# Performance work log

Measured on AMD Instinct MI355X. Metric: run time of the kernel, lower is better.

## Reference

```python
import jax, jax.numpy as jnp
import numpy as np

S, B, C, H, E, V, T = 196, 64, 1024, 1024, 512, 32000, 20


def setup_inputs() -> dict:
    key = jax.random.key(0)
    ks = jax.random.split(key, 16)

    def w(k, shape, fan_in):
        return (jax.random.normal(k, shape, jnp.float32) / np.sqrt(fan_in)).astype(jnp.float32)

    emb_W = w(ks[2], (V, E), E).at[0].set(0.0)  # padding_idx=0
    return {
        'ctx': jax.random.normal(ks[0], (S, B, C), jnp.float32),
        'y': jax.random.randint(ks[1], (T, B), 0, V, jnp.int32),
        'emb_W': emb_W,
        'att_ctx2ctx': w(ks[3], (C, C), C),
        'att_hid2ctx': w(ks[4], (H, C), H),
        'att_mlp': w(ks[5], (C,), C),
        'gru_W_ih': w(ks[6], (3 * H, E + C), E + C),
        'gru_b_ih': jnp.zeros((3 * H,), jnp.float32),
        'gru_W_hh': w(ks[7], (3 * H, H), H),
        'gru_b_hh': jnp.zeros((3 * H,), jnp.float32),
        'hid2out_W': w(ks[8], (E, H), H),
        'hid2out_b': jnp.zeros((E,), jnp.float32),
        'out_ctx_W': w(ks[9], (E, C), C),
        'out_ctx_b': jnp.zeros((E,), jnp.float32),
        'out2prob_W': w(ks[10], (V, E), E),
        'out2prob_b': jnp.zeros((V,), jnp.float32),
    }


def reference(ctx, y, emb_W, att_ctx2ctx, att_hid2ctx, att_mlp,
              gru_W_ih, gru_b_ih, gru_W_hh, gru_b_hh,
              hid2out_W, hid2out_b, out_ctx_W, out_ctx_b,
              out2prob_W, out2prob_b):
    hidden = gru_W_hh.shape[1]
    y_emb = emb_W[y]                                        # [T, B, E]
    ctx_proj = jnp.einsum('sbc,cm->sbm', ctx, att_ctx2ctx)  # precompute ctx2ctx(ctx)

    def gru_cell(x, h):
        gi = x @ gru_W_ih.T + gru_b_ih
        gh = h @ gru_W_hh.T + gru_b_hh
        i_r, i_z, i_n = jnp.split(gi, 3, axis=-1)
        h_r, h_z, h_n = jnp.split(gh, 3, axis=-1)
        r = jax.nn.sigmoid(i_r + h_r)
        z = jax.nn.sigmoid(i_z + h_z)
        n = jnp.tanh(i_n + r * h_n)
        return (1.0 - z) * n + z * h

    def step(h, inp):
        y_t, tgt = inp                                      # [B,E], [B]
        # MLP attention over source positions S
        scores = jnp.einsum('sbm,m->sb', jnp.tanh(ctx_proj + (h @ att_hid2ctx)[None]), att_mlp)
        alpha = jax.nn.softmax(scores, axis=0)              # [S, B]
        z_t = jnp.einsum('sb,sbc->bc', alpha, ctx)          # [B, C]
        ht = gru_cell(jnp.concatenate([y_t, z_t], axis=-1), h)
        logit = jnp.tanh(ht @ hid2out_W.T + hid2out_b)      # hid2out (tanh FF)
        logit = logit + y_t                                 # prev2out
        logit = logit + z_t @ out_ctx_W.T + out_ctx_b       # ctx2out
        log_p = jax.nn.log_softmax(jnp.tanh(logit) @ out2prob_W.T + out2prob_b, axis=-1)
        mask = (tgt != 0).astype(log_p.dtype)               # NLLLoss ignore_index=0, sum
        nll = -jnp.sum(jnp.take_along_axis(log_p, tgt[:, None], axis=1)[:, 0] * mask)
        return ht, nll

    h0 = jnp.zeros((y.shape[1], hidden), ctx.dtype)         # dec_init='zero'
    _, nlls = jax.lax.scan(step, h0, (y_emb[:-1], y[1:]))
    return jnp.sum(nlls)
```

## Files before the change

kernel.cpp:

```cpp
#include <hip/hip_runtime.h>
#include <math.h>

#define TS_ 19

typedef float f32x4 __attribute__((ext_vector_type(4)));
typedef short s16x8 __attribute__((ext_vector_type(8)));
typedef unsigned short us;
typedef unsigned char uc;

__device__ __forceinline__ float sigmoidf_(float x) { return 1.f / (1.f + __expf(-x)); }

__device__ __forceinline__ float fast_tanh(float x) {
    float ax = fabsf(x);
    float e = __expf(-2.f * ax);
    float r = (1.f - e) * __builtin_amdgcn_rcpf(1.f + e);
    return copysignf(r, x);
}

__device__ __forceinline__ us f2b(float x) {
    union { float f; unsigned u; } v; v.f = x;
    unsigned r = v.u + 0x7fffu + ((v.u >> 16) & 1u);
    return (us)(r >> 16);
}
__device__ __forceinline__ float b2f(us u) {
    union { unsigned u; float f; } v; v.u = ((unsigned)u) << 16; return v.f;
}
__device__ __forceinline__ uc f2e4m3(float x) {
    return (uc)(__builtin_amdgcn_cvt_pk_fp8_f32(x, 0.f, 0, false) & 0xff);
}

#define MFMA(a, b, c) __builtin_amdgcn_mfma_f32_16x16x32_bf16((a), (b), (c), 0, 0, 0)
#define MFMA8(a, b, c) __builtin_amdgcn_mfma_f32_16x16x32_fp8_fp8((a), (b), (c), 0, 0, 0)

__device__ __forceinline__ f32x4 zero4() { return (f32x4){0.f, 0.f, 0.f, 0.f}; }

__device__ __forceinline__ f32x4 wg16(const us* ap, const us* bp, int nk, f32x4 acc) {
#pragma unroll 4
    for (int k = 0; k < nk; k += 32)
        acc = MFMA(*(const s16x8*)(ap + k), *(const s16x8*)(bp + k), acc);
    return acc;
}

__device__ __forceinline__ void gload_lds16(const void* g, void* l) {
    __builtin_amdgcn_global_load_lds(
        (const __attribute__((address_space(1))) unsigned int*)g,
        (__attribute__((address_space(3))) unsigned int*)l, 16, 0, 0);
}

__global__ __launch_bounds__(256) void k_cvt(const float* __restrict__ in,
                                             us* __restrict__ out, long n) {
    long i = ((long)blockIdx.x * 256 + threadIdx.x) * 4;
    long stride = (long)gridDim.x * 1024;
    for (; i < n; i += stride) {
        float4 v = *(const float4*)(in + i);
        ushort4 o = { f2b(v.x), f2b(v.y), f2b(v.z), f2b(v.w) };
        *(ushort4*)(out + i) = o;
    }
}

__global__ __launch_bounds__(256) void k_cvt8(const float* __restrict__ in,
                                              uc* __restrict__ out, long n) {
    long i = ((long)blockIdx.x * 256 + threadIdx.x) * 8;
    long stride = (long)gridDim.x * 2048;
    for (; i < n; i += stride) {
        float4 v0 = *(const float4*)(in + i);
        float4 v1 = *(const float4*)(in + i + 4);
        int lo = __builtin_amdgcn_cvt_pk_fp8_f32(v0.x, v0.y, 0, false);
        lo = __builtin_amdgcn_cvt_pk_fp8_f32(v0.z, v0.w, lo, true);
        int hi = __builtin_amdgcn_cvt_pk_fp8_f32(v1.x, v1.y, 0, false);
        hi = __builtin_amdgcn_cvt_pk_fp8_f32(v1.z, v1.w, hi, true);
        int2 o = { lo, hi };
        *(int2*)(out + i) = o;
    }
}

__global__ void k_tcvt(const float* __restrict__ in, us* __restrict__ out) {
    __shared__ float tile[32][33];
    int bx = blockIdx.x * 32, by = blockIdx.y * 32;
    int x = threadIdx.x, y0 = threadIdx.y;
    for (int yy = y0; yy < 32; yy += 8) tile[yy][x] = in[(by + yy) * 1024 + bx + x];
    __syncthreads();
    for (int yy = y0; yy < 32; yy += 8) out[(bx + yy) * 1024 + by + x] = f2b(tile[x][yy]);
}

__global__ __launch_bounds__(256) void k_yemb(const int* __restrict__ y,
                                              const float* __restrict__ embW,
                                              us* __restrict__ xc) {
    int t = blockIdx.x >> 6, b = blockIdx.x & 63;
    int row = y[t * 64 + b];
    const float* src = embW + (long)row * 512;
    us* dst = xc + (long)(t * 64 + b) * 2560;
    for (int e = threadIdx.x; e < 512; e += 256) dst[e] = f2b(src[e]);
}

__global__ __launch_bounds__(256) void k_prepw(const float* __restrict__ Wih,
                                               const float* __restrict__ Whh,
                                               us* __restrict__ Wg) {
    int n = blockIdx.x, tid = threadIdx.x;
    int cl = n >> 10;
    if (cl < 2) {
        long base = (long)n * 2560;
        const float* wi = Wih + (long)n * 1536;
        const float* wh = Whh + (long)n * 1024;
        for (int k = tid; k < 1536; k += 256) Wg[base + k] = f2b(wi[k]);
        for (int k = tid; k < 1024; k += 256) Wg[base + 1536 + k] = f2b(wh[k]);
    } else if (cl == 2) {
        long base = 5242880L + (long)(n - 2048) * 1536;
        const float* wi = Wih + (long)n * 1536;
        for (int k = tid; k < 1536; k += 256) Wg[base + k] = f2b(wi[k]);
    } else {
        long base = 6815744L + (long)(n - 3072) * 1024;
        const float* wh = Whh + (long)(n - 1024) * 1024;
        for (int k = tid; k < 1024; k += 256) Wg[base + k] = f2b(wh[k]);
    }
}

__global__ __launch_bounds__(256) void k_gemm(const us* __restrict__ A,
                                              const us* __restrict__ Bt,
                                              us* __restrict__ Cb) {
    __shared__ us As[8192], Bs[8192];
    int tid = threadIdx.x, lane = tid & 63, w = tid >> 6;
    int mr = lane & 15, kb = lane >> 4;
    int bm = blockIdx.x % 98, bn = blockIdx.x / 98;
    long m0 = (long)bm * 128;
    int n0 = bn * 128;
    int wr = w >> 1, wc = w & 1;
    int srow = w * 32 + (lane >> 3);
    int ib = (lane & 7) * 16;

    f32x4 acc[4][4];
#pragma unroll
    for (int i = 0; i < 4; i++)
#pragma unroll
        for (int j = 0; j < 4; j++) acc[i][j] = zero4();

    for (int kt = 0; kt < 16; ++kt) {
        int k0 = kt * 64;
        __syncthreads();
#pragma unroll
        for (int c = 0; c < 4; ++c) {
            int r = srow + c * 8;
            int sw = (ib ^ ((r & 7) << 4)) >> 1;
            gload_lds16(A + (m0 + r) * 1024 + k0 + sw, &As[w * 2048 + c * 512]);
            gload_lds16(Bt + (long)(n0 + r) * 1024 + k0 + sw, &Bs[w * 2048 + c * 512]);
        }
        __syncthreads();
#pragma unroll
        for (int ks = 0; ks < 2; ++ks) {
            s16x8 af[4], bf[4];
#pragma unroll
            for (int mt = 0; mt < 4; ++mt) {
                int r = wr * 64 + mt * 16 + mr;
                af[mt] = *(const s16x8*)&As[(r * 128 + ((ks * 64 + kb * 16) ^ ((r & 7) << 4))) >> 1];
            }
#pragma unroll
            for (int nt = 0; nt < 4; ++nt) {
                int r = wc * 64 + nt * 16 + mr;
                bf[nt] = *(const s16x8*)&Bs[(r * 128 + ((ks * 64 + kb * 16) ^ ((r & 7) << 4))) >> 1];
            }
#pragma unroll
            for (int mt = 0; mt < 4; ++mt)
#pragma unroll
                for (int nt = 0; nt < 4; ++nt)
                    acc[mt][nt] = MFMA(af[mt], bf[nt], acc[mt][nt]);
        }
    }
#pragma unroll
    for (int mt = 0; mt < 4; ++mt)
#pragma unroll
        for (int nt = 0; nt < 4; ++nt)
#pragma unroll
            for (int j = 0; j < 4; ++j)
                Cb[(m0 + wr * 64 + mt * 16 + kb * 4 + j) * 1024 +
                   n0 + wc * 64 + nt * 16 + mr] = f2b(acc[mt][nt][j]);
}

__global__ __launch_bounds__(256) void k_hproj(const us* __restrict__ hcur,
                                               const us* __restrict__ attbf,
                                               float* __restrict__ hpp) {
    int tid = threadIdx.x, lane = tid & 63, w = tid >> 6;
    int vn0 = (blockIdx.x >> 1) * 16, kc = blockIdx.x & 1;
    int m0 = w * 16, mr = lane & 15, kb = lane >> 4;
    const us* ap = hcur + (long)(m0 + mr) * 1024 + kc * 512 + kb * 8;
    const us* bp = attbf + (long)(vn0 + mr) * 1024 + kc * 512 + kb * 8;
    f32x4 acc = wg16(ap, bp, 512, zero4());
#pragma unroll
    for (int j = 0; j < 4; ++j)
        hpp[(long)kc * 65536 + (long)(m0 + kb * 4 + j) * 1024 + vn0 + mr] = acc[j];
}

__global__ __launch_bounds__(1024) void k_scores(const us* __restrict__ cpb,
                                                 const float* __restrict__ hpp,
                                                 const float* __restrict__ mlp,
                                                 float* __restrict__ scores) {
    __shared__ float hp[1024];
    __shared__ float ml[1024];
    int tid = threadIdx.x;
    int b = blockIdx.x >> 2, sq = blockIdx.x & 3;
    hp[tid] = hpp[(long)b * 1024 + tid] + hpp[65536 + (long)b * 1024 + tid];
    ml[tid] = mlp[tid];
    __syncthreads();
    int wv = tid >> 6, lane = tid & 63;
    int s0 = sq * 49;
    for (int s = s0 + wv; s < s0 + 49; s += 16) {
        const us* cp = cpb + (long)(s * 64 + b) * 1024 + lane * 16;
        s16x8 c0 = *(const s16x8*)cp;
        s16x8 c1 = *(const s16x8*)(cp + 8);
        int e0 = lane * 16;
        float acc = 0.f;
#pragma unroll
        for (int j = 0; j < 8; ++j)
            acc += fast_tanh(b2f((us)c0[j]) + hp[e0 + j]) * ml[e0 + j];
#pragma unroll
        for (int j = 0; j < 8; ++j)
            acc += fast_tanh(b2f((us)c1[j]) + hp[e0 + 8 + j]) * ml[e0 + 8 + j];
#pragma unroll
        for (int off = 32; off; off >>= 1) acc += __shfl_xor(acc, off, 64);
        if (lane == 0) scores[b * 196 + s] = acc;
    }
}

__global__ __launch_bounds__(512) void k_z(const float* __restrict__ scores,
                                           const us* __restrict__ ctxbf,
                                           us* __restrict__ xc, int t) {
    __shared__ float red[512];
    __shared__ float als[196];
    __shared__ float zp[256];
    int tid = threadIdx.x, b = blockIdx.x >> 2, ch = blockIdx.x & 3;
    const float* sc = scores + b * 196;
    float lm = (tid < 196) ? sc[tid] : -1e30f;
    red[tid] = lm; __syncthreads();
    for (int st = 256; st; st >>= 1) { if (tid < st) red[tid] = fmaxf(red[tid], red[tid + st]); __syncthreads(); }
    float m = red[0]; __syncthreads();
    float ls = (tid < 196) ? __expf(sc[tid] - m) : 0.f;
    red[tid] = ls; __syncthreads();
    for (int st = 256; st; st >>= 1) { if (tid < st) red[tid] += red[tid + st]; __syncthreads(); }
    float inv = 1.f / red[0];
    if (tid < 196) als[tid] = ls * inv;
    __syncthreads();
    int c = ch * 256 + (tid & 255);
    int sh = tid >> 8;
    const us* cp = ctxbf + (long)b * 1024 + c;
    float a0 = 0.f;
    int sb = sh * 98;
#pragma unroll 4
    for (int s = sb; s < sb + 98; s += 2) {
        a0 += als[s] * b2f(cp[(long)s * 65536]) +
              als[s + 1] * b2f(cp[(long)(s + 1) * 65536]);
    }
    if (sh) zp[tid & 255] = a0;
    __syncthreads();
    if (!sh) {
        a0 += zp[tid & 255];
        xc[(long)(t * 64 + b) * 2560 + 512 + c] = f2b(a0);
    }
}

__global__ __launch_bounds__(512) void k_gruh2(us* __restrict__ xc,
                                               const us* __restrict__ Wg,
                                               const float* __restrict__ bih,
                                               const float* __restrict__ bhh,
                                               float* __restrict__ hf32,
                                               us* __restrict__ ht_all, int t) {
    __shared__ float lg[2048];
    int tid = threadIdx.x, lane = tid & 63, w = tid >> 6;
    int mr = lane & 15, kb = lane >> 4;
    int g = w >> 1, kh = w & 1;
    int mq = blockIdx.x & 3, jt = blockIdx.x >> 2;
    int m0 = mq * 16, j0 = jt * 16;
    const us* xr = xc + (long)t * 163840 + (long)(m0 + mr) * 2560;

    f32x4 acc = zero4();
    if (g == 0) {
        acc = wg16(xr + kh * 1280 + kb * 8,
                   Wg + (long)(j0 + mr) * 2560 + kh * 1280 + kb * 8, 1280, acc);
    } else if (g == 1) {
        acc = wg16(xr + kh * 1280 + kb * 8,
                   Wg + (long)(1024 + j0 + mr) * 2560 + kh * 1280 + kb * 8, 1280, acc);
    } else if (g == 2) {
        acc = wg16(xr + kh * 768 + kb * 8,
                   Wg + 5242880L + (long)(j0 + mr) * 1536 + kh * 768 + kb * 8, 768, acc);
    } else {
        acc = wg16(xr + 1536 + kh * 512 + kb * 8,
                   Wg + 6815744L + (long)(j0 + mr) * 1024 + kh * 512 + kb * 8, 512, acc);
    }
#pragma unroll
    for (int j = 0; j < 4; ++j)
        lg[(g * 2 + kh) * 256 + (kb * 4 + j) * 16 + mr] = acc[j];
    __syncthreads();

    if (tid < 256) {
        int ml = tid >> 4, jj = tid & 15;
        int b = m0 + ml, j = j0 + jj;
        float gr = lg[0 * 256 + ml * 16 + jj] + lg[1 * 256 + ml * 16 + jj];
        float gz = lg[2 * 256 + ml * 16 + jj] + lg[3 * 256 + ml * 16 + jj];
        float gi = lg[4 * 256 + ml * 16 + jj] + lg[5 * 256 + ml * 16 + jj];
        float gh = lg[6 * 256 + ml * 16 + jj] + lg[7 * 256 + ml * 16 + jj];
        float r  = sigmoidf_(gr + bih[j] + bhh[j]);
        float zz = sigmoidf_(gz + bih[1024 + j] + bhh[1024 + j]);
        float n  = fast_tanh(gi + bih[2048 + j] + r * (gh + bhh[2048 + j]));
        float h = (1.f - zz) * n + zz * hf32[b * 1024 + j];
        hf32[b * 1024 + j] = h;
        us hb = f2b(h);
        ht_all[(long)((t + 1) * 64 + b) * 1024 + j] = hb;
        if (t < TS_ - 1) xc[(long)((t + 1) * 64 + b) * 2560 + 1536 + j] = hb;
    }
}

__global__ __launch_bounds__(256) void k_outb(const us* __restrict__ ht_all,
                                              const us* __restrict__ xc,
                                              const us* __restrict__ h2obf,
                                              const float* __restrict__ h2ob,
                                              const us* __restrict__ octxbf,
                                              const float* __restrict__ octxb,
                                              us* __restrict__ obf_all,
                                              uc* __restrict__ obf8) {
    int tid = threadIdx.x, lane = tid & 63, w = tid >> 6;
    int mr = lane & 15, kb = lane >> 4;
    int m0 = blockIdx.x * 64;
    int n0 = blockIdx.y * 64;
    int e = n0 + w * 16 + mr;
    const us* bb1 = h2obf + (long)e * 1024 + kb * 8;
    const us* bb2 = octxbf + (long)e * 1024 + kb * 8;
    const us* ab1 = ht_all + (long)(64 + m0 + mr) * 1024 + kb * 8;
    const us* ab2 = xc + (long)(m0 + mr) * 2560 + 512 + kb * 8;

    f32x4 a1[4], a2[4];
#pragma unroll
    for (int i = 0; i < 4; i++) { a1[i] = zero4(); a2[i] = zero4(); }

#pragma unroll 2
    for (int k0 = 0; k0 < 1024; k0 += 32) {
        s16x8 b1 = *(const s16x8*)(bb1 + k0);
        s16x8 b2 = *(const s16x8*)(bb2 + k0);
#pragma unroll
        for (int mt = 0; mt < 4; ++mt) {
            a1[mt] = MFMA(*(const s16x8*)(ab1 + mt * 16384 + k0), b1, a1[mt]);
            a2[mt] = MFMA(*(const s16x8*)(ab2 + mt * 40960 + k0), b2, a2[mt]);
        }
    }
    float b1v = h2ob[e], b2v = octxb[e];
#pragma unroll
    for (int mt = 0; mt < 4; ++mt)
#pragma unroll
        for (int j = 0; j < 4; ++j) {
            long row = m0 + mt * 16 + kb * 4 + j;
            float ye = b2f(xc[row * 2560 + e]);
            float val = fast_tanh(fast_tanh(a1[mt][j] + b1v) + ye + a2[mt][j] + b2v);
            obf_all[(row << 9) + e] = f2b(val);
            obf8[(row << 9) + e] = f2e4m3(val);
        }
}

__global__ __launch_bounds__(256) void k_vocab8(const uc* __restrict__ obf8,
                                                const uc* __restrict__ o2p8,
                                                const float* __restrict__ o2pb,
                                                float* __restrict__ pm,
                                                float* __restrict__ ps) {
    __shared__ uc As[8192], Bs[8192];
    int tid = threadIdx.x, lane = tid & 63, w = tid >> 6;
    int mr = lane & 15, kb = lane >> 4;
    int xq = blockIdx.x & 7, idx = blockIdx.x >> 3;
    int nb = xq * 32 + idx / 10, mb = idx % 10;
    int m0 = mb * 128, n0 = nb * 128;
    int wr = w >> 1, wc = w & 1;
    int srow = w * 32 + (lane >> 2);
    int ib = (lane & 3) * 16;

    f32x4 acc[4][4];
#pragma unroll
    for (int i = 0; i < 4; i++)
#pragma unroll
        for (int j = 0; j < 4; j++) acc[i][j] = zero4();

    for (int kt = 0; kt < 8; ++kt) {
        int k0 = kt * 64;
        __syncthreads();
#pragma unroll
        for (int c = 0; c < 2; ++c) {
            int r = srow + c * 16;
            int sw = ib ^ ((r & 6) << 3);
            gload_lds16(obf8 + (long)(m0 + r) * 512 + k0 + sw, &As[w * 2048 + c * 1024]);
            gload_lds16(o2p8 + (long)(n0 + r) * 512 + k0 + sw, &Bs[w * 2048 + c * 1024]);
        }
        __syncthreads();
#pragma unroll
        for (int ks = 0; ks < 2; ++ks) {
            long af[4], bf[4];
#pragma unroll
            for (int mt = 0; mt < 4; ++mt) {
                int r = wr * 64 + mt * 16 + mr;
                af[mt] = *(const long*)&As[r * 64 + ((ks * 32 + kb * 8) ^ ((r & 6) << 3))];
            }
#pragma unroll
            for (int nt = 0; nt < 4; ++nt) {
                int r = wc * 64 + nt * 16 + mr;
                bf[nt] = *(const long*)&Bs[r * 64 + ((ks * 32 + kb * 8) ^ ((r & 6) << 3))];
            }
#pragma unroll
            for (int mt = 0; mt < 4; ++mt)
#pragma unroll
                for (int nt = 0; nt < 4; ++nt)
                    acc[mt][nt] = MFMA8(af[mt], bf[nt], acc[mt][nt]);
        }
    }

    int n0w = n0 + wc * 64;
    float bv[4];
#pragma unroll
    for (int nt = 0; nt < 4; ++nt) {
        int vn = n0w + nt * 16 + mr;
        bv[nt] = (vn < 32000) ? o2pb[vn] : -1e30f;
    }
#pragma unroll
    for (int mt = 0; mt < 4; ++mt)
#pragma unroll
        for (int j = 0; j < 4; ++j) {
            float x0 = acc[mt][0][j] + bv[0];
            float x1 = acc[mt][1][j] + bv[1];
            float x2 = acc[mt][2][j] + bv[2];
            float x3 = acc[mt][3][j] + bv[3];
            float m = fmaxf(fmaxf(x0, x1), fmaxf(x2, x3));
            float s = __expf(x0 - m) + __expf(x1 - m) + __expf(x2 - m) + __expf(x3 - m);
#pragma unroll
            for (int off = 1; off <= 8; off <<= 1) {
                float mo = __shfl_xor(m, off, 64), so = __shfl_xor(s, off, 64);
                float nm = fmaxf(m, mo);
                s = s * __expf(m - nm) + so * __expf(mo - nm);
                m = nm;
            }
            if (mr == 0) {
                int row = m0 + wr * 64 + mt * 16 + kb * 4 + j;
                pm[(long)(nb * 2 + wc) * 1280 + row] = m;
                ps[(long)(nb * 2 + wc) * 1280 + row] = s;
            }
        }
}

__global__ __launch_bounds__(64) void k_lseb(const float* __restrict__ pm,
                                             const float* __restrict__ ps,
                                             const us* __restrict__ obf_all,
                                             const float* __restrict__ o2pW,
                                             const float* __restrict__ o2pb,
                                             const int* __restrict__ y,
                                             float* __restrict__ out) {
    int r = blockIdx.x, lane = threadIdx.x;
    int t = r >> 6, b = r & 63;
    int tgt = y[(t + 1) * 64 + b];
    float m = -1e30f, s = 0.f;
    for (int p = lane; p < 512; p += 64) {
        float mi = pm[(long)p * 1280 + r], si = ps[(long)p * 1280 + r];
        float nm = fmaxf(m, mi);
        s = s * __expf(m - nm) + si * __expf(mi - nm);
        m = nm;
    }
#pragma unroll
    for (int off = 32; off; off >>= 1) {
        float mo = __shfl_xor(m, off, 64), so = __shfl_xor(s, off, 64);
        float nm = fmaxf(m, mo);
        s = s * __expf(m - nm) + so * __expf(mo - nm);
        m = nm;
    }
    float d = 0.f;
    const float* wr = o2pW + (long)tgt * 512;
#pragma unroll
    for (int k = 0; k < 8; ++k)
        d += b2f(obf_all[(long)r * 512 + lane + k * 64]) * wr[lane + k * 64];
#pragma unroll
    for (int off = 32; off; off >>= 1) d += __shfl_xor(d, off, 64);
    if (lane == 0 && tgt != 0)
        atomicAdd(out, (m + __logf(s)) - (d + o2pb[tgt]));
}

extern "C" void kernel_launch(void* const* d_in, const int* in_sizes, int n_in,
                              void* d_out, int out_size, void* d_ws, size_t ws_size,
                              hipStream_t stream) {
    const float* ctx     = (const float*)d_in[0];
    const int*   y       = (const int*)d_in[1];
    const float* embW    = (const float*)d_in[2];
    const float* att_c2c = (const float*)d_in[3];
    const float* att_h2c = (const float*)d_in[4];
    const float* mlp     = (const float*)d_in[5];
    const float* Wih     = (const float*)d_in[6];
    const float* bih     = (const float*)d_in[7];
    const float* Whh     = (const float*)d_in[8];
    const float* bhh     = (const float*)d_in[9];
    const float* h2oW    = (const float*)d_in[10];
    const float* h2ob    = (const float*)d_in[11];
    const float* octxW   = (const float*)d_in[12];
    const float* octxb   = (const float*)d_in[13];
    const float* o2pW    = (const float*)d_in[14];
    const float* o2pb    = (const float*)d_in[15];
    float* out = (float*)d_out;

    char* base = (char*)d_ws;
    us* ctxbf   = (us*)base; base += 25690112L;
    us* cpbf    = (us*)base; base += 25690112L;
    us* c2cT    = (us*)base; base += 2097152L;
    us* attbf   = (us*)base; base += 2097152L;
    us* Wg      = (us*)base; base += 15728640L;
    us* h2obf   = (us*)base; base += 1048576L;
    us* octxbf  = (us*)base; base += 1048576L;
    uc* o2p8    = (uc*)base; base += 16777216L;
    us* xc      = (us*)base; base += 6225920L;
    us* ht_all  = (us*)base; base += 2621440L;
    us* obf_all = (us*)base; base += 1310720L;
    uc* obf8    = (uc*)base; base += 655360L;
    float* hf32   = (float*)base; base += 262144L;
    float* hpp    = (float*)base; base += 524288L;
    float* scb    = (float*)base; base += 50176L;
    float* pm   = (float*)cpbf;
    float* ps   = pm + 655360L;

    (void)hipMemsetAsync(d_out, 0, sizeof(float), stream);
    (void)hipMemsetAsync(hf32, 0, 262144, stream);
    (void)hipMemsetAsync(ht_all, 0, 131072, stream);
    (void)hipMemsetAsync(obf_all + 1216L * 512, 0, 65536, stream);
    (void)hipMemsetAsync(obf8 + 1216L * 512, 0, 32768, stream);
    (void)hipMemsetAsync(o2p8 + 16384000L, 0, 393216, stream);
    (void)hipMemsetAsync(xc, 0, 6225920, stream);

    k_yemb<<<TS_ * 64, 256, 0, stream>>>(y, embW, xc);
    k_tcvt<<<dim3(32, 32), dim3(32, 8), 0, stream>>>(att_c2c, c2cT);
    k_tcvt<<<dim3(32, 32), dim3(32, 8), 0, stream>>>(att_h2c, attbf);
    k_cvt<<<2048, 256, 0, stream>>>(ctx, ctxbf, 12845056L);
    k_cvt<<<512, 256, 0, stream>>>(h2oW, h2obf, 524288L);
    k_cvt<<<512, 256, 0, stream>>>(octxW, octxbf, 524288L);
    k_cvt8<<<2048, 256, 0, stream>>>(o2pW, o2p8, 16384000L);
    k_prepw<<<4096, 256, 0, stream>>>(Wih, Whh, Wg);
    k_gemm<<<784, 256, 0, stream>>>(ctxbf, c2cT, cpbf);

    for (int t = 0; t < TS_; t++) {
        k_hproj<<<128, 256, 0, stream>>>(ht_all + (long)t * 65536, attbf, hpp);
        k_scores<<<256, 1024, 0, stream>>>(cpbf, hpp, mlp, scb);
        k_z<<<256, 512, 0, stream>>>(scb, ctxbf, xc, t);
        k_gruh2<<<256, 512, 0, stream>>>(xc, Wg, bih, bhh, hf32, ht_all, t);
    }

    k_outb<<<dim3(19, 8), 256, 0, stream>>>(ht_all, xc, h2obf, h2ob, octxbf, octxb,
                                            obf_all, obf8);
    k_vocab8<<<2560, 256, 0, stream>>>(obf8, o2p8, o2pb, pm, ps);
    k_lseb<<<1216, 64, 0, stream>>>(pm, ps, obf_all, o2pW, o2pb, y, out);
}
```

Baseline: 1.031 ms.

## Fuse attention scores, softmax and context sum into one kernel per step

Merges the score and context-weighted-sum kernels into a single kernel, so each block computes all 196 scores, does a wave-level softmax, and then sums over ctx for half the channels. This removes one launch per step and the global round trip for the scores. In exchange each batch row's scores are computed twice (once per channel half) and fewer blocks are launched (128 instead of 256), which lowers parallelism. It also remaps GRU blocks so that neighbouring j-tiles land on the same XCD, aiming for better L2 reuse of the weights.

After: 1.172 ms. 13.7% more time.

```diff
diff --git a/kernel.cpp b/kernel.cpp
--- a/kernel.cpp
+++ b/kernel.cpp
@@ -189,70 +189,84 @@
         hpp[(long)kc * 65536 + (long)(m0 + kb * 4 + j) * 1024 + vn0 + mr] = acc[j];
 }
 
-__global__ __launch_bounds__(1024) void k_scores(const us* __restrict__ cpb,
-                                                 const float* __restrict__ hpp,
-                                                 const float* __restrict__ mlp,
-                                                 float* __restrict__ scores) {
+__global__ __launch_bounds__(1024) void k_att2(const us* __restrict__ cpb,
+                                               const float* __restrict__ hpp,
+                                               const float* __restrict__ mlp,
+                                               const us* __restrict__ ctxbf,
+                                               us* __restrict__ xc, int t) {
     __shared__ float hp[1024];
     __shared__ float ml[1024];
+    __shared__ float scs[200];
+    __shared__ float als[200];
+    __shared__ float zp[3][512];
     int tid = threadIdx.x;
-    int b = blockIdx.x >> 2, sq = blockIdx.x & 3;
+    int b = blockIdx.x >> 1, chalf = blockIdx.x & 1;
+
     hp[tid] = hpp[(long)b * 1024 + tid] + hpp[65536 + (long)b * 1024 + tid];
     ml[tid] = mlp[tid];
     __syncthreads();
-    int wv = tid >> 6, lane = tid & 63;
-    int s0 = sq * 49;
-    for (int s = s0 + wv; s < s0 + 49; s += 16) {
-        const us* cp = cpb + (long)(s * 64 + b) * 1024 + lane * 16;
-        s16x8 c0 = *(const s16x8*)cp;
-        s16x8 c1 = *(const s16x8*)(cp + 8);
-        int e0 = lane * 16;
-        float acc = 0.f;
-#pragma unroll
-        for (int j = 0; j < 8; ++j)
-            acc += fast_tanh(b2f((us)c0[j]) + hp[e0 + j]) * ml[e0 + j];
-#pragma unroll
-        for (int j = 0; j < 8; ++j)
-            acc += fast_tanh(b2f((us)c1[j]) + hp[e0 + 8 + j]) * ml[e0 + 8 + j];
-#pragma unroll
-        for (int off = 32; off; off >>= 1) acc += __shfl_xor(acc, off, 64);
-        if (lane == 0) scores[b * 196 + s] = acc;
-    }
-}
-
-__global__ __launch_bounds__(512) void k_z(const float* __restrict__ scores,
-                                           const us* __restrict__ ctxbf,
-                                           us* __restrict__ xc, int t) {
-    __shared__ float red[512];
-    __shared__ float als[196];
-    __shared__ float zp[256];
-    int tid = threadIdx.x, b = blockIdx.x >> 2, ch = blockIdx.x & 3;
-    const float* sc = scores + b * 196;
-    float lm = (tid < 196) ? sc[tid] : -1e30f;
-    red[tid] = lm; __syncthreads();
-    for (int st = 256; st; st >>= 1) { if (tid < st) red[tid] = fmaxf(red[tid], red[tid + st]); __syncthreads(); }
-    float m = red[0]; __syncthreads();
-    float ls = (tid < 196) ? __expf(sc[tid] - m) : 0.f;
-    red[tid] = ls; __syncthreads();
-    for (int st = 256; st; st >>= 1) { if (tid < st) red[tid] += red[tid + st]; __syncthreads(); }
-    float inv = 1.f / red[0];
-    if (tid < 196) als[tid] = ls * inv;
+
+    {
+        int wv = tid >> 6, lane = tid & 63;
+        for (int s = wv; s < 196; s += 16) {
+            const us* cp = cpb + (long)(s * 64 + b) * 1024 + lane * 16;
+            s16x8 c0 = *(const s16x8*)cp;
+            s16x8 c1 = *(const s16x8*)(cp + 8);
+            int e0 = lane * 16;
+            float acc = 0.f;
+#pragma unroll
+            for (int j = 0; j < 8; ++j)
+                acc += fast_tanh(b2f((us)c0[j]) + hp[e0 + j]) * ml[e0 + j];
+#pragma unroll
+            for (int j = 0; j < 8; ++j)
+                acc += fast_tanh(b2f((us)c1[j]) + hp[e0 + 8 + j]) * ml[e0 + 8 + j];
+#pragma unroll
+            for (int off = 32; off; off >>= 1) acc += __shfl_xor(acc, off, 64);
+            if (lane == 0) scs[s] = acc;
+        }
+    }
     __syncthreads();
-    int c = ch * 256 + (tid & 255);
-    int sh = tid >> 8;
-    const us* cp = ctxbf + (long)b * 1024 + c;
-    float a0 = 0.f;
-    int sb = sh * 98;
-#pragma unroll 4
-    for (int s = sb; s < sb + 98; s += 2) {
-        a0 += als[s] * b2f(cp[(long)s * 65536]) +
-              als[s + 1] * b2f(cp[(long)(s + 1) * 65536]);
-    }
-    if (sh) zp[tid & 255] = a0;
+
+    if (tid < 64) {
+        int lane = tid;
+        float v0 = scs[lane], v1 = scs[lane + 64], v2 = scs[lane + 128];
+        float v3 = (lane < 4) ? scs[192 + lane] : -1e30f;
+        float m = fmaxf(fmaxf(v0, v1), fmaxf(v2, v3));
+#pragma unroll
+        for (int off = 32; off; off >>= 1) m = fmaxf(m, __shfl_xor(m, off, 64));
+        float pI = __expf(v0 - m) + __expf(v1 - m) + __expf(v2 - m);
+        if (lane < 4) pI += __expf(v3 - m);
+#pragma unroll
+        for (int off = 32; off; off >>= 1) pI += __shfl_xor(pI, off, 64);
+        float inv = 1.f / pI;
+        als[lane] = __expf(v0 - m) * inv;
+        als[lane + 64] = __expf(v1 - m) * inv;
+        als[lane + 128] = __expf(v2 - m) * inv;
+        if (lane < 4) als[192 + lane] = __expf(v3 - m) * inv;
+    }
     __syncthreads();
-    if (!sh) {
-        a0 += zp[tid & 255];
-        xc[(long)(t * 64 + b) * 2560 + 512 + c] = f2b(a0);
+
+    {
+        int cp2 = tid & 255, sq = tid >> 8;
+        int c = chalf * 512 + cp2 * 2;
+        const us* cptr = ctxbf + (long)b * 1024 + c;
+        float a0 = 0.f, a1 = 0.f;
+        int sb = sq * 49;
+#pragma unroll 7
+        for (int s = sb; s < sb + 49; ++s) {
+            float al = als[s];
+            ushort2 v = *(const ushort2*)(cptr + (long)s * 65536);
+            a0 += al * b2f(v.x);
+            a1 += al * b2f(v.y);
+        }
+        if (sq) { zp[sq - 1][cp2 * 2] = a0; zp[sq - 1][cp2 * 2 + 1] = a1; }
+        __syncthreads();
+        if (sq == 0) {
+            a0 += zp[0][cp2 * 2] + zp[1][cp2 * 2] + zp[2][cp2 * 2];
+            a1 += zp[0][cp2 * 2 + 1] + zp[1][cp2 * 2 + 1] + zp[2][cp2 * 2 + 1];
+            ushort2 o = { f2b(a0), f2b(a1) };
+            *(ushort2*)(xc + (long)(t * 64 + b) * 2560 + 512 + c) = o;
+        }
     }
 }
 
@@ -266,7 +280,8 @@
     int tid = threadIdx.x, lane = tid & 63, w = tid >> 6;
     int mr = lane & 15, kb = lane >> 4;
     int g = w >> 1, kh = w & 1;
-    int mq = blockIdx.x & 3, jt = blockIdx.x >> 2;
+    int xcd = blockIdx.x & 7, idx = blockIdx.x >> 3;
+    int jt = xcd * 8 + (idx >> 2), mq = idx & 3;
     int m0 = mq * 16, j0 = jt * 16;
     const us* xr = xc + (long)t * 163840 + (long)(m0 + mr) * 2560;
 
@@ -508,7 +523,6 @@
     uc* obf8    = (uc*)base; base += 655360L;
     float* hf32   = (float*)base; base += 262144L;
     float* hpp    = (float*)base; base += 524288L;
-    float* scb    = (float*)base; base += 50176L;
     float* pm   = (float*)cpbf;
     float* ps   = pm + 655360L;
 
@@ -532,8 +546,7 @@
 
     for (int t = 0; t < TS_; t++) {
         k_hproj<<<128, 256, 0, stream>>>(ht_all + (long)t * 65536, attbf, hpp);
-        k_scores<<<256, 1024, 0, stream>>>(cpbf, hpp, mlp, scb);
-        k_z<<<256, 512, 0, stream>>>(scb, ctxbf, xc, t);
+        k_att2<<<128, 1024, 0, stream>>>(cpbf, hpp, mlp, ctxbf, xc, t);
         k_gruh2<<<256, 512, 0, stream>>>(xc, Wg, bih, bhh, hf32, ht_all, t);
     }
 
```

## Fuse all preprocessing conversions and memsets into one multi-role kernel

Applied to the files above, without the earlier changes.

Seven memsets and eight conversion or transpose launches are replaced by a single k_prep kernel whose block ranges each handle one job: casting ctx and weights, the fp8 vocab weights, the GRU weight packing, the embedding gather, the two transposes and the zeroing of padding buffers. The full 6 MB memset of xc is narrowed to zeroing only the h-column slice that k_prep itself does not write. This aims to cut launch and serialization overhead and let the independent jobs overlap. Separately, k_gruh2 remaps blockIdx so each XCD handles a contiguous range of output columns, intended to improve L2 locality for the weight reads.

After: 982.7 us. 1.05x faster.

```diff
diff --git a/kernel.cpp b/kernel.cpp
--- a/kernel.cpp
+++ b/kernel.cpp
@@ -47,71 +47,126 @@
         (__attribute__((address_space(3))) unsigned int*)l, 16, 0, 0);
 }
 
-__global__ __launch_bounds__(256) void k_cvt(const float* __restrict__ in,
-                                             us* __restrict__ out, long n) {
-    long i = ((long)blockIdx.x * 256 + threadIdx.x) * 4;
-    long stride = (long)gridDim.x * 1024;
-    for (; i < n; i += stride) {
-        float4 v = *(const float4*)(in + i);
-        ushort4 o = { f2b(v.x), f2b(v.y), f2b(v.z), f2b(v.w) };
-        *(ushort4*)(out + i) = o;
-    }
-}
-
-__global__ __launch_bounds__(256) void k_cvt8(const float* __restrict__ in,
-                                              uc* __restrict__ out, long n) {
-    long i = ((long)blockIdx.x * 256 + threadIdx.x) * 8;
-    long stride = (long)gridDim.x * 2048;
-    for (; i < n; i += stride) {
-        float4 v0 = *(const float4*)(in + i);
-        float4 v1 = *(const float4*)(in + i + 4);
-        int lo = __builtin_amdgcn_cvt_pk_fp8_f32(v0.x, v0.y, 0, false);
-        lo = __builtin_amdgcn_cvt_pk_fp8_f32(v0.z, v0.w, lo, true);
-        int hi = __builtin_amdgcn_cvt_pk_fp8_f32(v1.x, v1.y, 0, false);
-        hi = __builtin_amdgcn_cvt_pk_fp8_f32(v1.z, v1.w, hi, true);
-        int2 o = { lo, hi };
-        *(int2*)(out + i) = o;
-    }
-}
-
-__global__ void k_tcvt(const float* __restrict__ in, us* __restrict__ out) {
+__global__ __launch_bounds__(256) void k_prep(
+    const float* __restrict__ ctx, us* __restrict__ ctxbf,
+    const float* __restrict__ o2pW, uc* __restrict__ o2p8,
+    const float* __restrict__ Wih, const float* __restrict__ Whh, us* __restrict__ Wg,
+    const float* __restrict__ h2oW, us* __restrict__ h2obf,
+    const float* __restrict__ octxW, us* __restrict__ octxbf,
+    const float* __restrict__ att_c2c, us* __restrict__ c2cT,
+    const float* __restrict__ att_h2c, us* __restrict__ attbf,
+    const int* __restrict__ y, const float* __restrict__ embW, us* __restrict__ xc,
+    float* __restrict__ hf32, us* __restrict__ ht_all,
+    us* __restrict__ obf_all, uc* __restrict__ obf8, float* __restrict__ out) {
     __shared__ float tile[32][33];
-    int bx = blockIdx.x * 32, by = blockIdx.y * 32;
-    int x = threadIdx.x, y0 = threadIdx.y;
-    for (int yy = y0; yy < 32; yy += 8) tile[yy][x] = in[(by + yy) * 1024 + bx + x];
-    __syncthreads();
-    for (int yy = y0; yy < 32; yy += 8) out[(bx + yy) * 1024 + by + x] = f2b(tile[x][yy]);
-}
-
-__global__ __launch_bounds__(256) void k_yemb(const int* __restrict__ y,
-                                              const float* __restrict__ embW,
-                                              us* __restrict__ xc) {
-    int t = blockIdx.x >> 6, b = blockIdx.x & 63;
-    int row = y[t * 64 + b];
-    const float* src = embW + (long)row * 512;
-    us* dst = xc + (long)(t * 64 + b) * 2560;
-    for (int e = threadIdx.x; e < 512; e += 256) dst[e] = f2b(src[e]);
-}
-
-__global__ __launch_bounds__(256) void k_prepw(const float* __restrict__ Wih,
-                                               const float* __restrict__ Whh,
-                                               us* __restrict__ Wg) {
-    int n = blockIdx.x, tid = threadIdx.x;
-    int cl = n >> 10;
-    if (cl < 2) {
-        long base = (long)n * 2560;
-        const float* wi = Wih + (long)n * 1536;
-        const float* wh = Whh + (long)n * 1024;
-        for (int k = tid; k < 1536; k += 256) Wg[base + k] = f2b(wi[k]);
-        for (int k = tid; k < 1024; k += 256) Wg[base + 1536 + k] = f2b(wh[k]);
-    } else if (cl == 2) {
-        long base = 5242880L + (long)(n - 2048) * 1536;
-        const float* wi = Wih + (long)n * 1536;
-        for (int k = tid; k < 1536; k += 256) Wg[base + k] = f2b(wi[k]);
+    int bid = blockIdx.x, tid = threadIdx.x;
+    const int4 z4 = {0, 0, 0, 0};
+
+    if (bid < 1024) {
+        for (long i = ((long)bid * 256 + tid) * 4; i < 12845056L; i += 1048576L) {
+            float4 v = *(const float4*)(ctx + i);
+            ushort4 o = { f2b(v.x), f2b(v.y), f2b(v.z), f2b(v.w) };
+            *(ushort4*)(ctxbf + i) = o;
+        }
+    } else if (bid < 1792) {
+        for (long i = ((long)(bid - 1024) * 256 + tid) * 8; i < 16384000L;
+             i += 1572864L) {
+            float4 v0 = *(const float4*)(o2pW + i);
+            float4 v1 = *(const float4*)(o2pW + i + 4);
+            int lo = __builtin_amdgcn_cvt_pk_fp8_f32(v0.x, v0.y, 0, false);
+            lo = __builtin_amdgcn_cvt_pk_fp8_f32(v0.z, v0.w, lo, true);
+            int hi = __builtin_amdgcn_cvt_pk_fp8_f32(v1.x, v1.y, 0, false);
+            hi = __builtin_amdgcn_cvt_pk_fp8_f32(v1.z, v1.w, hi, true);
+            int2 o = { lo, hi };
+            *(int2*)(o2p8 + i) = o;
+        }
+    } else if (bid < 2816) {
+        for (int n = bid - 1792; n < 4096; n += 1024) {
+            int cl = n >> 10;
+            if (cl < 2) {
+                long bb = (long)n * 2560;
+                const float* wi = Wih + (long)n * 1536;
+                const float* wh = Whh + (long)n * 1024;
+                for (int k = tid; k < 1536; k += 256) Wg[bb + k] = f2b(wi[k]);
+                for (int k = tid; k < 1024; k += 256) Wg[bb + 1536 + k] = f2b(wh[k]);
+            } else if (cl == 2) {
+                long bb = 5242880L + (long)(n - 2048) * 1536;
+                const float* wi = Wih + (long)n * 1536;
+                for (int k = tid; k < 1536; k += 256) Wg[bb + k] = f2b(wi[k]);
+            } else {
+                long bb = 6815744L + (long)(n - 3072) * 1024;
+                const float* wh = Whh + (long)(n - 1024) * 1024;
+                for (int k = tid; k < 1024; k += 256) Wg[bb + k] = f2b(wh[k]);
+            }
+        }
+    } else if (bid < 2880) {
+        for (long i = ((long)(bid - 2816) * 256 + tid) * 4; i < 524288L; i += 65536L) {
+            float4 v = *(const float4*)(h2oW + i);
+            ushort4 o = { f2b(v.x), f2b(v.y), f2b(v.z), f2b(v.w) };
+            *(ushort4*)(h2obf + i) = o;
+        }
+    } else if (bid < 2944) {
+        for (long i = ((long)(bid - 2880) * 256 + tid) * 4; i < 524288L; i += 65536L) {
+            float4 v = *(const float4*)(octxW + i);
+            ushort4 o = { f2b(v.x), f2b(v.y), f2b(v.z), f2b(v.w) };
+            *(ushort4*)(octxbf + i) = o;
+        }
+    } else if (bid < 3072) {
+        for (int r = bid - 2944; r < 1216; r += 128) {
+            int row = y[r];
+            const float* src = embW + (long)row * 512;
+            us* dst = xc + (long)r * 2560;
+            for (int e = tid; e < 512; e += 256) dst[e] = f2b(src[e]);
+        }
+    } else if (bid < 4096) {
+        int g = bid - 3072;
+        int bx = (g & 31) * 32, by = (g >> 5) * 32;
+        int x = tid & 31, y0 = tid >> 5;
+        for (int yy = y0; yy < 32; yy += 8) tile[yy][x] = att_c2c[(by + yy) * 1024 + bx + x];
+        __syncthreads();
+        for (int yy = y0; yy < 32; yy += 8) c2cT[(bx + yy) * 1024 + by + x] = f2b(tile[x][yy]);
+    } else if (bid < 5120) {
+        int g = bid - 4096;
+        int bx = (g & 31) * 32, by = (g >> 5) * 32;
+        int x = tid & 31, y0 = tid >> 5;
+        for (int yy = y0; yy < 32; yy += 8) tile[yy][x] = att_h2c[(by + yy) * 1024 + bx + x];
+        __syncthreads();
+        for (int yy = y0; yy < 32; yy += 8) attbf[(bx + yy) * 1024 + by + x] = f2b(tile[x][yy]);
     } else {
-        long base = 6815744L + (long)(n - 3072) * 1024;
-        const float* wh = Whh + (long)(n - 1024) * 1024;
-        for (int k = tid; k < 1024; k += 256) Wg[base + k] = f2b(wh[k]);
+        int zb = bid - 5120;
+        if (zb < 32) {
+            int4* p = (int4*)hf32;
+            int i = zb * 256 + tid;
+            p[i] = z4; p[i + 8192] = z4;
+        } else if (zb < 40) {
+            int4* p = (int4*)ht_all;
+            int i = (zb - 32) * 256 + tid;
+#pragma unroll
+            for (int k = 0; k < 4; ++k) p[i + k * 2048] = z4;
+        } else if (zb < 56) {
+            int cbase = (zb - 40) * 4;
+#pragma unroll
+            for (int c = 0; c < 4; ++c) {
+                ushort4* p = (ushort4*)(xc + (long)(cbase + c) * 2560 + 1536);
+                ushort4 o = {0, 0, 0, 0};
+                p[tid] = o;
+            }
+        } else if (zb < 64) {
+            int4* p = (int4*)(obf_all + 1216L * 512);
+            int i = (zb - 56) * 256 + tid;
+            p[i] = z4; p[i + 2048] = z4;
+        } else if (zb < 68) {
+            int4* p = (int4*)(obf8 + 1216L * 512);
+            int i = (zb - 64) * 256 + tid;
+            p[i] = z4; p[i + 1024] = z4;
+        } else if (zb < 92) {
+            int4* p = (int4*)(o2p8 + 16384000L);
+            int i = (zb - 68) * 256 + tid;
+#pragma unroll
+            for (int k = 0; k < 4; ++k) p[i + k * 6144] = z4;
+        } else {
+            if (tid == 0) out[0] = 0.f;
+        }
     }
 }
 
@@ -266,7 +321,8 @@
     int tid = threadIdx.x, lane = tid & 63, w = tid >> 6;
     int mr = lane & 15, kb = lane >> 4;
     int g = w >> 1, kh = w & 1;
-    int mq = blockIdx.x & 3, jt = blockIdx.x >> 2;
+    int xcd = blockIdx.x & 7, idx = blockIdx.x >> 3;
+    int jt = xcd * 8 + (idx >> 2), mq = idx & 3;
     int m0 = mq * 16, j0 = jt * 16;
     const us* xr = xc + (long)t * 163840 + (long)(m0 + mr) * 2560;
 
@@ -512,22 +568,10 @@
     float* pm   = (float*)cpbf;
     float* ps   = pm + 655360L;
 
-    (void)hipMemsetAsync(d_out, 0, sizeof(float), stream);
-    (void)hipMemsetAsync(hf32, 0, 262144, stream);
-    (void)hipMemsetAsync(ht_all, 0, 131072, stream);
-    (void)hipMemsetAsync(obf_all + 1216L * 512, 0, 65536, stream);
-    (void)hipMemsetAsync(obf8 + 1216L * 512, 0, 32768, stream);
-    (void)hipMemsetAsync(o2p8 + 16384000L, 0, 393216, stream);
-    (void)hipMemsetAsync(xc, 0, 6225920, stream);
-
-    k_yemb<<<TS_ * 64, 256, 0, stream>>>(y, embW, xc);
-    k_tcvt<<<dim3(32, 32), dim3(32, 8), 0, stream>>>(att_c2c, c2cT);
-    k_tcvt<<<dim3(32, 32), dim3(32, 8), 0, stream>>>(att_h2c, attbf);
-    k_cvt<<<2048, 256, 0, stream>>>(ctx, ctxbf, 12845056L);
-    k_cvt<<<512, 256, 0, stream>>>(h2oW, h2obf, 524288L);
-    k_cvt<<<512, 256, 0, stream>>>(octxW, octxbf, 524288L);
-    k_cvt8<<<2048, 256, 0, stream>>>(o2pW, o2p8, 16384000L);
-    k_prepw<<<4096, 256, 0, stream>>>(Wih, Whh, Wg);
+    k_prep<<<5213, 256, 0, stream>>>(ctx, ctxbf, o2pW, o2p8, Wih, Whh, Wg,
+                                     h2oW, h2obf, octxW, octxbf,
+                                     att_c2c, c2cT, att_h2c, attbf,
+                                     y, embW, xc, hf32, ht_all, obf_all, obf8, out);
     k_gemm<<<784, 256, 0, stream>>>(ctxbf, c2cT, cpbf);
 
     for (int t = 0; t < TS_; t++) {
```
